# Optimization experiments

Hardware: AMD Instinct MI355X
Metric: run time of the kernel (lower is better)

## Reference

```python
import jax, jax.numpy as jnp
import numpy as np

N_NODES = 100000
N_EDGES = 1200000
N_GRAPHS = 2048
NUM_SHAPE, NUM_COLOR, NUM_CLASS = 8, 8, 10
MAX_POS, EMB, HID = 20, 16, 64
IN_DIM = 3 * EMB  # 48


def setup_inputs() -> dict:
    key = jax.random.key(0)
    ks = jax.random.split(key, 14)
    x = jax.random.randint(ks[0], (N_NODES, 3), 0, NUM_SHAPE)
    edge_index = jax.random.randint(ks[1], (2, N_EDGES), 0, N_NODES)
    batch = jnp.sort(jax.random.randint(ks[2], (N_NODES,), 0, N_GRAPHS))
    s = 0.1
    return {
        'x': x, 'edge_index': edge_index, 'batch': batch, 'num_graphs': N_GRAPHS,
        'shape_emb': jax.random.normal(ks[3], (NUM_SHAPE, EMB)) * s,
        'color_emb': jax.random.normal(ks[4], (NUM_COLOR, EMB)) * s,
        'pos_emb': jax.random.normal(ks[5], (MAX_POS, EMB)) * s,
        'W1_l': jax.random.normal(ks[6], (IN_DIM, HID)) * s,
        'W1_r': jax.random.normal(ks[7], (IN_DIM, HID)) * s,
        'b1': jnp.zeros((HID,)),
        'W2_l': jax.random.normal(ks[8], (HID, HID)) * s,
        'W2_r': jax.random.normal(ks[9], (HID, HID)) * s,
        'b2': jnp.zeros((HID,)),
        'Wc': jax.random.normal(ks[10], (HID, NUM_CLASS)) * s,
        'bc': jnp.zeros((NUM_CLASS,)),
    }


def _sage(h, src, dst, W_l, W_r, b, n_nodes):
    # mean-aggregate neighbor features x[src] into dst, then linear combine with root
    agg = jax.ops.segment_sum(h[src], dst, num_segments=n_nodes)
    deg = jax.ops.segment_sum(jnp.ones((src.shape[0],), h.dtype), dst, num_segments=n_nodes)
    mean = agg / jnp.maximum(deg, 1.0)[:, None]
    return mean @ W_l + h @ W_r + b


def reference(x, edge_index, batch, num_graphs, shape_emb, color_emb, pos_emb,
              W1_l, W1_r, b1, W2_l, W2_r, b2, Wc, bc):
    n_nodes = x.shape[0]
    shp = shape_emb[x[:, 0]]
    col = color_emb[x[:, 1]]
    pos = pos_emb[jnp.clip(x[:, 2], 0, MAX_POS - 1)]
    h = jnp.concatenate([shp, col, pos], axis=-1)  # [N, 48]
    src, dst = edge_index[0], edge_index[1]
    h = jax.nn.relu(_sage(h, src, dst, W1_l, W1_r, b1, n_nodes))
    h = jax.nn.relu(_sage(h, src, dst, W2_l, W2_r, b2, n_nodes))
    # global mean pool per graph
    gsum = jax.ops.segment_sum(h, batch, num_segments=num_graphs)
    gcnt = jax.ops.segment_sum(jnp.ones((n_nodes,), h.dtype), batch, num_segments=num_graphs)
    hg = gsum / jnp.maximum(gcnt, 1.0)[:, None]
    return hg @ Wc + bc
```

## Files before the change

### kernel.cpp

```cpp
#include <hip/hip_runtime.h>

#define N_NODES 100000
#define N_EDGES 1200000
#define N_GRAPHS 2048
#define NBKT 36
#define CAPA 16
#define CAPB 32
#define NBUCK 500
#define DPB 200
#define BCAP 4864
#define TILE 4096

typedef unsigned int uint;
typedef unsigned short ushort;
typedef __attribute__((ext_vector_type(8))) short short8;
typedef __attribute__((ext_vector_type(4))) float f32x4;

__device__ __forceinline__ int atomAddI(int* p, int v) {
    return __hip_atomic_fetch_add(p, v, __ATOMIC_RELAXED, __HIP_MEMORY_SCOPE_AGENT);
}
__device__ __forceinline__ int clampPos(int v) { return min(max(v, 0), 19); }
__device__ __forceinline__ uint f2bf(float f) {
    uint b = __float_as_uint(f);
    return (b + 0x7fffu + ((b >> 16) & 1u)) >> 16;
}
__device__ __forceinline__ int bucketOf(int d) {
    return (int)(((uint)((d >> 3) * 5243)) >> 17);
}

__global__ __launch_bounds__(256) void k_init(
    const int* __restrict__ x,
    const float* __restrict__ se, const float* __restrict__ ce,
    const float* __restrict__ pe,
    const float* __restrict__ W1l, const float* __restrict__ W1r,
    const float* __restrict__ W2l, const float* __restrict__ W2r,
    float* __restrict__ W1eff, float* __restrict__ Rtab,
    ushort* __restrict__ WstkT,
    int* __restrict__ gcur, int* __restrict__ xpk) {
    int t = blockIdx.x * 256 + threadIdx.x;
    if (t < NBKT * 64) {
        int bkt = t / 64, j = t % 64;
        const float* erow; int f0;
        if (bkt < 8)       { erow = se + bkt * 16;        f0 = 0;  }
        else if (bkt < 16) { erow = ce + (bkt - 8) * 16;  f0 = 16; }
        else               { erow = pe + (bkt - 16) * 16; f0 = 32; }
        float al = 0.f, ar = 0.f;
        #pragma unroll
        for (int f = 0; f < 16; ++f) {
            al = fmaf(erow[f], W1l[(f0 + f) * 64 + j], al);
            ar = fmaf(erow[f], W1r[(f0 + f) * 64 + j], ar);
        }
        W1eff[t] = al; Rtab[t] = ar;
    }
    if (t < 64 * 128) {
        int col = t >> 7, k = t & 127;
        float wv = (k < 64) ? W2r[k * 64 + col] : W2l[(k - 64) * 64 + col];
        WstkT[col * 128 + k] = (ushort)f2bf(wv);
    }
    if (t < NBUCK) gcur[t] = 0;
    for (int i = t; i < N_NODES; i += 256 * 256) {
        int xs = x[i * 3 + 0], xc = x[i * 3 + 1], xp = clampPos(x[i * 3 + 2]);
        xpk[i] = xs | (xc << 8) | (xp << 16);
    }
}

__global__ __launch_bounds__(256) void k_bin(const int* __restrict__ ei,
                                             int* __restrict__ gcur,
                                             int2* __restrict__ binned) {
    __shared__ int hist[NBUCK], offs[NBUCK], runc[NBUCK], gbase[NBUCK];
    __shared__ int2 stag[TILE];
    int tid = threadIdx.x;
    int tile_base = blockIdx.x * TILE;
    int tile_n = min(TILE, N_EDGES - tile_base);
    int n4 = tile_n >> 2;
    const int4* s4p = (const int4*)(ei + tile_base);
    const int4* d4p = (const int4*)(ei + N_EDGES + tile_base);

    for (int t = tid; t < NBUCK; t += 256) hist[t] = 0;
    __syncthreads();
    for (int k = tid; k < n4; k += 256) {
        int4 d4 = d4p[k];
        #pragma unroll
        for (int i = 0; i < 4; ++i) atomicAdd(&hist[bucketOf((&d4.x)[i])], 1);
    }
    __syncthreads();
    if (tid < 64) {
        int carry = 0;
        for (int c = 0; c < 8; ++c) {
            int idx = c * 64 + tid;
            int v = (idx < NBUCK) ? hist[idx] : 0;
            int orig = v;
            #pragma unroll
            for (int o = 1; o < 64; o <<= 1) {
                int u = __shfl_up(v, o);
                if (tid >= o) v += u;
            }
            if (idx < NBUCK) offs[idx] = carry + v - orig;
            carry += __shfl(v, 63);
        }
    }
    __syncthreads();
    for (int t = tid; t < NBUCK; t += 256) runc[t] = offs[t];
    __syncthreads();
    for (int k = tid; k < n4; k += 256) {
        int4 d4 = d4p[k];
        int4 s4 = s4p[k];
        #pragma unroll
        for (int i = 0; i < 4; ++i) {
            int b = bucketOf((&d4.x)[i]);
            int pos = atomicAdd(&runc[b], 1);
            stag[pos] = make_int2((&s4.x)[i], (&d4.x)[i]);
        }
    }
    __syncthreads();
    for (int t = tid; t < NBUCK; t += 256) gbase[t] = atomAddI(&gcur[t], hist[t]);
    __syncthreads();
    for (int i = tid; i < tile_n; i += 256) {
        int2 p = stag[i];
        int b = bucketOf(p.y);
        int o = gbase[b] + (i - offs[b]);
        if (o < BCAP) binned[(size_t)b * BCAP + o] = p;
    }
}

__global__ __launch_bounds__(256) void k_place(const int2* __restrict__ binned,
                                               const int* __restrict__ gcur,
                                               int* __restrict__ cursor,
                                               int* __restrict__ slabA,
                                               int* __restrict__ slabB) {
    __shared__ int lslab[DPB][CAPA + CAPB];
    __shared__ int lcur[DPB];
    int b = blockIdx.x;
    int tid = threadIdx.x;
    if (tid < DPB) lcur[tid] = 0;
    __syncthreads();
    int n = min(gcur[b], BCAP);
    const int2* in = binned + (size_t)b * BCAP;
    for (int i = tid; i < n; i += 256) {
        int2 p = in[i];
        int local = p.y - b * DPB;
        int slot = atomicAdd(&lcur[local], 1);
        if (slot < CAPA + CAPB) lslab[local][slot] = p.x;
    }
    __syncthreads();
    for (int i = tid; i < DPB * CAPA; i += 256)
        slabA[b * DPB * CAPA + i] = lslab[i >> 4][i & 15];
    for (int i = tid; i < DPB * CAPB; i += 256)
        slabB[b * DPB * CAPB + i] = lslab[i >> 5][CAPA + (i & 31)];
    if (tid < DPB) cursor[b * DPB + tid] = lcur[tid];
}

__device__ __forceinline__ int slabAt(const int* __restrict__ slabA,
                                      const int* __restrict__ slabB,
                                      int row, int idx) {
    return (idx < CAPA) ? slabA[row * CAPA + idx] : slabB[row * CAPB + idx - CAPA];
}

__global__ __launch_bounds__(256) void k_layer1(
    const int* __restrict__ xpk, const int* __restrict__ cursor,
    const int* __restrict__ slabA, const int* __restrict__ slabB,
    const float* __restrict__ W1eff, const float* __restrict__ Rtab,
    const float* __restrict__ b1, uint* __restrict__ AbU) {
    __shared__ float sW[NBKT * 64];
    __shared__ float sR[NBKT * 64];
    __shared__ float sb[64];
    __shared__ int   sx[16];
    for (int i = threadIdx.x; i < NBKT * 64; i += 256) { sW[i] = W1eff[i]; sR[i] = Rtab[i]; }
    if (threadIdx.x < 64) sb[threadIdx.x] = b1[threadIdx.x];
    int row0 = blockIdx.x * 16;
    if (threadIdx.x < 16) sx[threadIdx.x] = xpk[row0 + threadIdx.x];
    __syncthreads();
    int wave = threadIdx.x >> 6, j = threadIdx.x & 63;
    for (int rr = 0; rr < 4; ++rr) {
        int r = wave * 4 + rr;
        int row = row0 + r;
        int deg = cursor[row];
        int m = min(deg, CAPA + CAPB);
        int xs = -1, xc = -1, xp = -1;
        if (j < m) {
            int p = xpk[slabAt(slabA, slabB, row, j)];
            xs = p & 0xff; xc = (p >> 8) & 0xff; xp = p >> 16;
        }
        float acc = 0.f;
        #pragma unroll
        for (int b = 0; b < 8; ++b) {
            float cs = (float)__popcll(__ballot(xs == b));
            float cc = (float)__popcll(__ballot(xc == b));
            acc = fmaf(cs, sW[b * 64 + j], acc);
            acc = fmaf(cc, sW[(8 + b) * 64 + j], acc);
        }
        #pragma unroll
        for (int b = 0; b < 20; ++b) {
            float cp = (float)__popcll(__ballot(xp == b));
            acc = fmaf(cp, sW[(16 + b) * 64 + j], acc);
        }
        int p0 = sx[r];
        int xs0 = p0 & 0xff, xc0 = (p0 >> 8) & 0xff, xp0 = p0 >> 16;
        float self = sR[xs0 * 64 + j] + sR[(8 + xc0) * 64 + j] + sR[(16 + xp0) * 64 + j];
        float v = fmaxf(acc / fmaxf((float)deg, 1.0f) + self + sb[j], 0.0f);
        uint rb = f2bf(v);
        uint nxt = __shfl_down(rb, 1);
        if ((j & 1) == 0) AbU[(size_t)row * 64 + (j >> 1)] = rb | (nxt << 16);
    }
}

__global__ __launch_bounds__(256) void k_gather(
    uint* __restrict__ AbU, const int* __restrict__ cursor,
    const int* __restrict__ slabA, const int* __restrict__ slabB) {
    int gid = blockIdx.x * 256 + threadIdx.x;
    int wid = gid >> 6;
    int lane = threadIdx.x & 63;
    int half = lane >> 5, l = lane & 31;
    int row = wid * 2 + half;
    if (row >= N_NODES) return;
    int deg = cursor[row];
    int m = min(deg, CAPA + CAPB);
    int nb0 = (l < m)      ? slabAt(slabA, slabB, row, l)      : 0;
    int nb1 = (l + 32 < m) ? slabB[row * CAPB + l + 32 - CAPA] : 0;
    float ax = 0.f, ay = 0.f;
    int d = 0;
    for (; d + 2 <= m; d += 2) {
        int s0 = __shfl((d < 32) ? nb0 : nb1, (half << 5) | (d & 31));
        int s1 = __shfl((d + 1 < 32) ? nb0 : nb1, (half << 5) | ((d + 1) & 31));
        uint v0 = AbU[(size_t)s0 * 64 + l];
        uint v1 = AbU[(size_t)s1 * 64 + l];
        ax += __uint_as_float(v0 << 16) + __uint_as_float(v1 << 16);
        ay += __uint_as_float(v0 & 0xffff0000u) + __uint_as_float(v1 & 0xffff0000u);
    }
    if (d < m) {
        int s = __shfl((d < 32) ? nb0 : nb1, (half << 5) | (d & 31));
        uint v = AbU[(size_t)s * 64 + l];
        ax += __uint_as_float(v << 16);
        ay += __uint_as_float(v & 0xffff0000u);
    }
    float inv = 1.0f / fmaxf((float)deg, 1.0f);
    AbU[(size_t)row * 64 + 32 + l] = f2bf(ax * inv) | (f2bf(ay * inv) << 16);
}

__global__ __launch_bounds__(256) void k_gemm(
    const uint* __restrict__ AbU, const ushort* __restrict__ WstkT,
    const float* __restrict__ b2, float* __restrict__ h2) {
    int w = threadIdx.x >> 6, lane = threadIdx.x & 63;
    int lo16 = lane & 15, hi4 = lane >> 4;
    short8 bfr[4][4];
    #pragma unroll
    for (int nb = 0; nb < 4; ++nb) {
        #pragma unroll
        for (int kb = 0; kb < 4; ++kb)
            bfr[nb][kb] = *(const short8*)(WstkT + (nb * 16 + lo16) * 128 + kb * 32 + hi4 * 8);
    }
    float bb[4];
    #pragma unroll
    for (int nb = 0; nb < 4; ++nb) bb[nb] = b2[nb * 16 + lo16];

    int row0 = blockIdx.x * 64 + w * 16;
    int arow = min(row0 + lo16, N_NODES - 1);
    const short8* Arow = (const short8*)(AbU + (size_t)arow * 64);
    short8 a8[4];
    #pragma unroll
    for (int kb = 0; kb < 4; ++kb) a8[kb] = Arow[kb * 4 + hi4];

    f32x4 acc[4] = {{0,0,0,0},{0,0,0,0},{0,0,0,0},{0,0,0,0}};
    #pragma unroll
    for (int kb = 0; kb < 4; ++kb) {
        #pragma unroll
        for (int nb = 0; nb < 4; ++nb)
            acc[nb] = __builtin_amdgcn_mfma_f32_16x16x32_bf16(a8[kb], bfr[nb][kb], acc[nb], 0, 0, 0);
    }
    #pragma unroll
    for (int nb = 0; nb < 4; ++nb) {
        #pragma unroll
        for (int r = 0; r < 4; ++r) {
            int orow = row0 + hi4 * 4 + r;
            if (orow < N_NODES)
                h2[(size_t)orow * 64 + nb * 16 + lo16] = fmaxf(acc[nb][r] + bb[nb], 0.f);
        }
    }
}

__device__ __forceinline__ int lowerBound(const int* __restrict__ b, int n, int v) {
    int lo = 0, hi = n;
    while (lo < hi) { int mid = (lo + hi) >> 1; if (b[mid] < v) lo = mid + 1; else hi = mid; }
    return lo;
}

__global__ __launch_bounds__(256) void k_pool_final(
    const float* __restrict__ h2, const int* __restrict__ batch,
    const float* __restrict__ Wc, const float* __restrict__ bc,
    float* __restrict__ out) {
    int g = blockIdx.x * 4 + (threadIdx.x >> 6);
    if (g >= N_GRAPHS) return;
    int j = threadIdx.x & 63;
    int lo = lowerBound(batch, N_NODES, g);
    int hi = lowerBound(batch, N_NODES, g + 1);
    float a0 = 0.f, a1 = 0.f, a2 = 0.f, a3 = 0.f;
    int n = lo;
    for (; n + 4 <= hi; n += 4) {
        a0 += h2[(size_t)n * 64 + j];
        a1 += h2[(size_t)(n + 1) * 64 + j];
        a2 += h2[(size_t)(n + 2) * 64 + j];
        a3 += h2[(size_t)(n + 3) * 64 + j];
    }
    for (; n < hi; ++n) a0 += h2[(size_t)n * 64 + j];
    float mean = ((a0 + a1) + (a2 + a3)) / fmaxf((float)(hi - lo), 1.0f);
    #pragma unroll
    for (int c = 0; c < 10; ++c) {
        float p = mean * Wc[j * 10 + c];
        #pragma unroll
        for (int off = 32; off >= 1; off >>= 1) p += __shfl_down(p, off);
        if (j == 0) out[g * 10 + c] = p + bc[c];
    }
}

extern "C" void kernel_launch(void* const* d_in, const int* in_sizes, int n_in,
                              void* d_out, int out_size, void* d_ws, size_t ws_size,
                              hipStream_t stream) {
    const int* x     = (const int*)d_in[0];
    const int* ei    = (const int*)d_in[1];
    const int* batch = (const int*)d_in[2];
    const float* se  = (const float*)d_in[4];
    const float* ce  = (const float*)d_in[5];
    const float* pe  = (const float*)d_in[6];
    const float* W1l = (const float*)d_in[7];
    const float* W1r = (const float*)d_in[8];
    const float* b1  = (const float*)d_in[9];
    const float* W2l = (const float*)d_in[10];
    const float* W2r = (const float*)d_in[11];
    const float* b2  = (const float*)d_in[12];
    const float* Wc  = (const float*)d_in[13];
    const float* bc  = (const float*)d_in[14];

    float* ws    = (float*)d_ws;
    uint*  AbU   = (uint*)ws;
    float* h2    = ws + 6400000;
    int2*  binned= (int2*)ws;
    int*   slabA = (int*)(ws + 12800000);
    int*   slabB = (int*)(ws + 14400000);
    int*   cursor= (int*)(ws + 17600000);
    int*   xpk   = (int*)(ws + 17700000);
    float* W1eff = ws + 17800000;
    float* Rtab  = ws + 17803000;
    ushort* WstkT= (ushort*)(ws + 17806000);
    int*   gcur  = (int*)(ws + 17812000);

    k_init<<<256, 256, 0, stream>>>(x, se, ce, pe, W1l, W1r, W2l, W2r,
                                    W1eff, Rtab, WstkT, gcur, xpk);
    k_bin<<<(N_EDGES + TILE - 1) / TILE, 256, 0, stream>>>(ei, gcur, binned);
    k_place<<<NBUCK, 256, 0, stream>>>(binned, gcur, cursor, slabA, slabB);
    k_layer1<<<N_NODES / 16, 256, 0, stream>>>(xpk, cursor, slabA, slabB, W1eff, Rtab, b1, AbU);
    k_gather<<<12500, 256, 0, stream>>>(AbU, cursor, slabA, slabB);
    k_gemm<<<(N_NODES + 63) / 64, 256, 0, stream>>>(AbU, WstkT, b2, h2);
    k_pool_final<<<(N_GRAPHS + 3) / 4, 256, 0, stream>>>(h2, batch, Wc, bc, (float*)d_out);
}
```

Measured before the change: 147.5 us.

## Compute layer-1 via shared-memory histogram counts and bf16 MFMA

Layer 1 previously counted neighbour categories with per-bucket wave ballots (36 ballots per row) and accumulated against fp32 tables held in shared memory. It now builds a per-row count vector in shared memory with atomics, adds one-hot self and bias entries, and multiplies it by a precomputed bf16 combined weight matrix (left, right and bias, padded to K=96) with three 16x16x32 MFMA instructions. This removes the serial ballot loop and the per-block loads of the 18 KB weight tables. In exchange, the scaled counts and weights are rounded to bf16, which adds precision error, and the shared-memory atomics may contend.

```diff
diff --git a/kernel.cpp b/kernel.cpp
--- a/kernel.cpp
+++ b/kernel.cpp
@@ -3,7 +3,6 @@
 #define N_NODES 100000
 #define N_EDGES 1200000
 #define N_GRAPHS 2048
-#define NBKT 36
 #define CAPA 16
 #define CAPB 32
 #define NBUCK 500
@@ -33,24 +32,29 @@
     const float* __restrict__ se, const float* __restrict__ ce,
     const float* __restrict__ pe,
     const float* __restrict__ W1l, const float* __restrict__ W1r,
+    const float* __restrict__ b1,
     const float* __restrict__ W2l, const float* __restrict__ W2r,
-    float* __restrict__ W1eff, float* __restrict__ Rtab,
-    ushort* __restrict__ WstkT,
+    ushort* __restrict__ WLt, ushort* __restrict__ WstkT,
     int* __restrict__ gcur, int* __restrict__ xpk) {
     int t = blockIdx.x * 256 + threadIdx.x;
-    if (t < NBKT * 64) {
-        int bkt = t / 64, j = t % 64;
-        const float* erow; int f0;
-        if (bkt < 8)       { erow = se + bkt * 16;        f0 = 0;  }
-        else if (bkt < 16) { erow = ce + (bkt - 8) * 16;  f0 = 16; }
-        else               { erow = pe + (bkt - 16) * 16; f0 = 32; }
-        float al = 0.f, ar = 0.f;
-        #pragma unroll
-        for (int f = 0; f < 16; ++f) {
-            al = fmaf(erow[f], W1l[(f0 + f) * 64 + j], al);
-            ar = fmaf(erow[f], W1r[(f0 + f) * 64 + j], ar);
-        }
-        W1eff[t] = al; Rtab[t] = ar;
+    if (t < 64 * 96) {
+        int col = t / 96, k = t - (t / 96) * 96;
+        float v = 0.f;
+        if (k < 72) {
+            int bkt = (k < 36) ? k : (k - 36);
+            const float* erow; int f0;
+            if (bkt < 8)       { erow = se + bkt * 16;        f0 = 0;  }
+            else if (bkt < 16) { erow = ce + (bkt - 8) * 16;  f0 = 16; }
+            else               { erow = pe + (bkt - 16) * 16; f0 = 32; }
+            const float* W = (k < 36) ? W1l : W1r;
+            float a = 0.f;
+            #pragma unroll
+            for (int f = 0; f < 16; ++f) a = fmaf(erow[f], W[(f0 + f) * 64 + col], a);
+            v = a;
+        } else if (k == 72) {
+            v = b1[col];
+        }
+        WLt[t] = (ushort)f2bf(v);
     }
     if (t < 64 * 128) {
         int col = t >> 7, k = t & 127;
@@ -159,48 +163,61 @@
 __global__ __launch_bounds__(256) void k_layer1(
     const int* __restrict__ xpk, const int* __restrict__ cursor,
     const int* __restrict__ slabA, const int* __restrict__ slabB,
-    const float* __restrict__ W1eff, const float* __restrict__ Rtab,
-    const float* __restrict__ b1, uint* __restrict__ AbU) {
-    __shared__ float sW[NBKT * 64];
-    __shared__ float sR[NBKT * 64];
-    __shared__ float sb[64];
-    __shared__ int   sx[16];
-    for (int i = threadIdx.x; i < NBKT * 64; i += 256) { sW[i] = W1eff[i]; sR[i] = Rtab[i]; }
-    if (threadIdx.x < 64) sb[threadIdx.x] = b1[threadIdx.x];
+    const ushort* __restrict__ WLt, uint* __restrict__ AbU) {
+    __shared__ int    cnt[16][104];
+    __shared__ ushort scnt[16][104];
+    __shared__ float  sinv[16];
+    __shared__ int    sdeg[16];
+    int tid = threadIdx.x;
     int row0 = blockIdx.x * 16;
-    if (threadIdx.x < 16) sx[threadIdx.x] = xpk[row0 + threadIdx.x];
-    __syncthreads();
-    int wave = threadIdx.x >> 6, j = threadIdx.x & 63;
-    for (int rr = 0; rr < 4; ++rr) {
-        int r = wave * 4 + rr;
-        int row = row0 + r;
-        int deg = cursor[row];
-        int m = min(deg, CAPA + CAPB);
-        int xs = -1, xc = -1, xp = -1;
-        if (j < m) {
-            int p = xpk[slabAt(slabA, slabB, row, j)];
-            xs = p & 0xff; xc = (p >> 8) & 0xff; xp = p >> 16;
-        }
-        float acc = 0.f;
-        #pragma unroll
-        for (int b = 0; b < 8; ++b) {
-            float cs = (float)__popcll(__ballot(xs == b));
-            float cc = (float)__popcll(__ballot(xc == b));
-            acc = fmaf(cs, sW[b * 64 + j], acc);
-            acc = fmaf(cc, sW[(8 + b) * 64 + j], acc);
-        }
-        #pragma unroll
-        for (int b = 0; b < 20; ++b) {
-            float cp = (float)__popcll(__ballot(xp == b));
-            acc = fmaf(cp, sW[(16 + b) * 64 + j], acc);
-        }
-        int p0 = sx[r];
-        int xs0 = p0 & 0xff, xc0 = (p0 >> 8) & 0xff, xp0 = p0 >> 16;
-        float self = sR[xs0 * 64 + j] + sR[(8 + xc0) * 64 + j] + sR[(16 + xp0) * 64 + j];
-        float v = fmaxf(acc / fmaxf((float)deg, 1.0f) + self + sb[j], 0.0f);
-        uint rb = f2bf(v);
+    for (int i = tid; i < 16 * 104; i += 256) cnt[i / 104][i % 104] = 0;
+    if (tid < 16) {
+        int dg = cursor[row0 + tid];
+        sdeg[tid] = min(dg, CAPA + CAPB);
+        sinv[tid] = 1.0f / fmaxf((float)dg, 1.0f);
+    }
+    __syncthreads();
+    for (int i = tid; i < 16 * 48; i += 256) {
+        int r = i / 48, idx = i - r * 48;
+        if (idx < sdeg[r]) {
+            int p = xpk[slabAt(slabA, slabB, row0 + r, idx)];
+            atomicAdd(&cnt[r][p & 0xff], 1);
+            atomicAdd(&cnt[r][8 + ((p >> 8) & 0xff)], 1);
+            atomicAdd(&cnt[r][16 + (p >> 16)], 1);
+        }
+    }
+    if (tid < 16) {
+        int p0 = xpk[row0 + tid];
+        cnt[tid][36 + (p0 & 0xff)] = 1;
+        cnt[tid][44 + ((p0 >> 8) & 0xff)] = 1;
+        cnt[tid][52 + (p0 >> 16)] = 1;
+        cnt[tid][72] = 1;
+    }
+    __syncthreads();
+    for (int i = tid; i < 16 * 96; i += 256) {
+        int r = i / 96, k = i - r * 96;
+        float v = (float)cnt[r][k];
+        if (k < 36) v *= sinv[r];
+        scnt[r][k] = (ushort)f2bf(v);
+    }
+    __syncthreads();
+    int w = tid >> 6, lane = tid & 63;
+    int lo16 = lane & 15, hi4 = lane >> 4;
+    f32x4 acc = {0.f, 0.f, 0.f, 0.f};
+    #pragma unroll
+    for (int ks = 0; ks < 3; ++ks) {
+        short8 a8 = *(const short8*)(&scnt[lo16][ks * 32 + hi4 * 8]);
+        short8 b8 = *(const short8*)(WLt + (w * 16 + lo16) * 96 + ks * 32 + hi4 * 8);
+        acc = __builtin_amdgcn_mfma_f32_16x16x32_bf16(a8, b8, acc, 0, 0, 0);
+    }
+    #pragma unroll
+    for (int r = 0; r < 4; ++r) {
+        uint rb = f2bf(fmaxf(acc[r], 0.0f));
         uint nxt = __shfl_down(rb, 1);
-        if ((j & 1) == 0) AbU[(size_t)row * 64 + (j >> 1)] = rb | (nxt << 16);
+        if ((lo16 & 1) == 0) {
+            int node = row0 + hi4 * 4 + r;
+            AbU[(size_t)node * 64 + ((w * 16 + lo16) >> 1)] = rb | (nxt << 16);
+        }
     }
 }
 
@@ -338,16 +355,15 @@
     int*   slabB = (int*)(ws + 14400000);
     int*   cursor= (int*)(ws + 17600000);
     int*   xpk   = (int*)(ws + 17700000);
-    float* W1eff = ws + 17800000;
-    float* Rtab  = ws + 17803000;
     ushort* WstkT= (ushort*)(ws + 17806000);
-    int*   gcur  = (int*)(ws + 17812000);
-
-    k_init<<<256, 256, 0, stream>>>(x, se, ce, pe, W1l, W1r, W2l, W2r,
-                                    W1eff, Rtab, WstkT, gcur, xpk);
+    ushort* WLt  = (ushort*)(ws + 17810100);
+    int*   gcur  = (int*)(ws + 17814000);
+
+    k_init<<<256, 256, 0, stream>>>(x, se, ce, pe, W1l, W1r, b1, W2l, W2r,
+                                    WLt, WstkT, gcur, xpk);
     k_bin<<<(N_EDGES + TILE - 1) / TILE, 256, 0, stream>>>(ei, gcur, binned);
     k_place<<<NBUCK, 256, 0, stream>>>(binned, gcur, cursor, slabA, slabB);
-    k_layer1<<<N_NODES / 16, 256, 0, stream>>>(xpk, cursor, slabA, slabB, W1eff, Rtab, b1, AbU);
+    k_layer1<<<N_NODES / 16, 256, 0, stream>>>(xpk, cursor, slabA, slabB, WLt, AbU);
     k_gather<<<12500, 256, 0, stream>>>(AbU, cursor, slabA, slabB);
     k_gemm<<<(N_NODES + 63) / 64, 256, 0, stream>>>(AbU, WstkT, b2, h2);
     k_pool_final<<<(N_GRAPHS + 3) / 4, 256, 0, stream>>>(h2, batch, Wc, bc, (float*)d_out);
```

After: 128.9 us. 1.14x faster.
